# Kernel tuning notes

Measured on AMD Instinct MI355X. Metric: run time of the kernel, lower is better.

Reference implementation:

```python
import jax, jax.numpy as jnp
import numpy as np

V, D, H, NL = 30000, 512, 8, 6
DH = D // H
B, L = 4, 1024
EPS = 1e-5


def setup_inputs() -> dict:
    key = jax.random.key(0)
    ks = jax.random.split(key, 16)
    s = 0.02
    n = lambda k, shape: jax.random.normal(k, shape, jnp.float32) * s
    return {
        'ids': jax.random.randint(ks[0], (B, L), 0, V),
        'embed': n(ks[1], (V, D)),
        'pos_enc': jax.random.normal(ks[2], (1, 1024, D), jnp.float32),
        'rg_w': n(ks[3], (NL, 4, D)), 'rg_b': jnp.zeros((NL, 4), jnp.float32),
        'qkv_w': n(ks[4], (NL, 3 * D, D)), 'qkv_b': jnp.zeros((NL, 3 * D), jnp.float32),
        'out_w': n(ks[5], (NL, D, D)), 'out_b': jnp.zeros((NL, D), jnp.float32),
        'phase_w': n(ks[6], (NL, H, D)), 'phase_b': jnp.zeros((NL, H), jnp.float32),
        'ff1_w': n(ks[7], (NL, 4 * D, D)), 'ff1_b': jnp.zeros((NL, 4 * D), jnp.float32),
        'ff2_w': n(ks[8], (NL, D, 4 * D)), 'ff2_b': jnp.zeros((NL, D), jnp.float32),
        'n1_s': jnp.ones((NL, D), jnp.float32), 'n1_b': jnp.zeros((NL, D), jnp.float32),
        'n2_s': jnp.ones((NL, D), jnp.float32), 'n2_b': jnp.zeros((NL, D), jnp.float32),
        'bnd_w1': n(ks[9], (D, D)), 'bnd_b1': jnp.zeros((D,), jnp.float32),
        'bnd_w2': n(ks[10], (1, D)), 'bnd_b2': jnp.zeros((1,), jnp.float32),
        'head_w': n(ks[11], (V, D)),
    }


def _ln(x, s, b):
    m = x.mean(-1, keepdims=True)
    v = ((x - m) ** 2).mean(-1, keepdims=True)
    return (x - m) * jax.lax.rsqrt(v + EPS) * s + b


def _block(x, p):
    rgw, rgb, qw, qb, ow, ob, pw, pb, f1w, f1b, f2w, f2b, s1, b1, s2, b2 = p
    Bc, Lc, _ = x.shape
    rg = jax.nn.sigmoid(x @ rgw.T + rgb)                       # [B,L,4]
    xm = x * (1.0 + rg.mean(-1, keepdims=True))
    h = _ln(xm, s1, b1)                                        # norm1(x_modulated)
    qkv = (h @ qw.T + qb).reshape(Bc, Lc, 3, H, DH)
    q, k, v = [jnp.transpose(qkv[:, :, i], (0, 2, 1, 3)) for i in range(3)]  # [B,H,L,dh]
    attn = jnp.einsum('bhid,bhjd->bhij', q, k) / (float(DH) ** 0.5)
    phase = jnp.transpose(h @ pw.T + pb, (0, 2, 1))            # [B,H,L]
    bias = -(phase[..., :, None] - phase[..., None, :]) ** 2   # [B,H,L,L]
    attn = jax.nn.softmax(attn + bias, axis=-1)
    ao = jnp.einsum('bhij,bhjd->bhid', attn, v)
    ao = jnp.transpose(ao, (0, 2, 1, 3)).reshape(Bc, Lc, D) @ ow.T + ob
    x = _ln(x + ao, s1, b1)
    ff = jax.nn.gelu(x @ f1w.T + f1b, approximate=False) @ f2w.T + f2b
    x = _ln(x + ff, s2, b2)
    return x, rg


def reference(ids, embed, pos_enc, rg_w, rg_b, qkv_w, qkv_b, out_w, out_b,
              phase_w, phase_b, ff1_w, ff1_b, ff2_w, ff2_b,
              n1_s, n1_b, n2_s, n2_b, bnd_w1, bnd_b1, bnd_w2, bnd_b2, head_w):
    Lc = ids.shape[1]
    x = embed[ids] + pos_enc[:, :Lc, :]
    layer_params = (rg_w, rg_b, qkv_w, qkv_b, out_w, out_b, phase_w, phase_b,
                    ff1_w, ff1_b, ff2_w, ff2_b, n1_s, n1_b, n2_s, n2_b)
    x, rgs = jax.lax.scan(_block, x, layer_params)
    gate = jax.nn.sigmoid((jnp.tanh(x @ bnd_w1.T + bnd_b1) @ bnd_w2.T + bnd_b2)[..., 0])
    logits = (x * gate[..., None]) @ head_w.T
    return logits, gate, rgs[-1]
```

## Files before the change

kernel.cpp:

```cpp
#include <hip/hip_runtime.h>
#include <math.h>

#define D 512
#define NH 8
#define DH 64
#define NL 6
#define Bsz 4
#define Lseq 1024
#define BL 4096
#define Vocab 30000
#define EPS 1e-5f

typedef __attribute__((ext_vector_type(8))) short s8v;
typedef __attribute__((ext_vector_type(4))) float f32x4;
typedef __attribute__((ext_vector_type(4))) float f4v;

__device__ __forceinline__ float sigmoidf_(float x) { return 1.0f / (1.0f + expf(-x)); }

__device__ __forceinline__ short f2bf(float f) {
  union { float f; unsigned u; } v; v.f = f;
  return (short)((v.u + 0x7FFFu + ((v.u >> 16) & 1u)) >> 16);
}
__device__ __forceinline__ float bf2f(short s) {
  union { unsigned u; float f; } v; v.u = ((unsigned)(unsigned short)s) << 16;
  return v.f;
}

__device__ __forceinline__ void gload16(const void* g, void* l) {
  __builtin_amdgcn_global_load_lds(
      (const __attribute__((address_space(1))) void*)g,
      (__attribute__((address_space(3))) void*)l, 16, 0, 0);
}

__device__ __forceinline__ float act_apply(float v, int act) {
  if (act == 1) return 0.5f * v * (1.0f + erff(v * 0.7071067811865475f));
  if (act == 2) return tanhf(v);
  return v;
}

__global__ void f2bf6_kernel(
    const float* __restrict__ s0, short* __restrict__ d0, int n0,
    const float* __restrict__ s1, short* __restrict__ d1, int n1,
    const float* __restrict__ s2, short* __restrict__ d2, int n2,
    const float* __restrict__ s3, short* __restrict__ d3, int n3,
    const float* __restrict__ s4, short* __restrict__ d4, int n4,
    const float* __restrict__ s5, short* __restrict__ d5, int n5) {
  long i = ((long)blockIdx.x * 256 + threadIdx.x) * 8;
  const float* s; short* d;
  if (i < n0) { s = s0; d = d0; }
  else {
    i -= n0;
    if (i < n1) { s = s1; d = d1; }
    else {
      i -= n1;
      if (i < n2) { s = s2; d = d2; }
      else {
        i -= n2;
        if (i < n3) { s = s3; d = d3; }
        else {
          i -= n3;
          if (i < n4) { s = s4; d = d4; }
          else { i -= n4; if (i >= n5) return; s = s5; d = d5; }
        }
      }
    }
  }
  float4 a = *(const float4*)(s + i);
  float4 b = *(const float4*)(s + i + 4);
  s8v o;
  o[0] = f2bf(a.x); o[1] = f2bf(a.y); o[2] = f2bf(a.z); o[3] = f2bf(a.w);
  o[4] = f2bf(b.x); o[5] = f2bf(b.y); o[6] = f2bf(b.z); o[7] = f2bf(b.w);
  *(s8v*)(d + i) = o;
}

__global__ void embed_kernel(const int* __restrict__ ids, const float* __restrict__ emb,
                             const float* __restrict__ pos, float* __restrict__ x) {
  int tok = blockIdx.x;
  int l = tok & (Lseq - 1);
  int id = ids[tok];
  const float4* e = (const float4*)(emb + (size_t)id * D);
  const float4* p = (const float4*)(pos + (size_t)l * D);
  float4* o = (float4*)(x + (size_t)tok * D);
  float4 a = e[threadIdx.x], b = p[threadIdx.x];
  o[threadIdx.x] = make_float4(a.x + b.x, a.y + b.y, a.z + b.z, a.w + b.w);
}

__global__ __launch_bounds__(256) void rg_ln_kernel(
    const float* __restrict__ x, const float* __restrict__ rgw, const float* __restrict__ rgb,
    const float* __restrict__ sc, const float* __restrict__ bi,
    const float* __restrict__ pw, const float* __restrict__ pb,
    short* __restrict__ h, float* __restrict__ phase, float* __restrict__ rg_out) {
  __shared__ float smg[4][4];
  __shared__ float sms[4][2];
  __shared__ float smp[4][8];
  int tok = blockIdx.x, t = threadIdx.x, wid = t >> 6, lane = t & 63;
  const float* xr = x + (size_t)tok * D;
  float x0 = xr[t], x1 = xr[t + 256];
  float p0 = x0 * rgw[t]        + x1 * rgw[t + 256];
  float p1 = x0 * rgw[512 + t]  + x1 * rgw[512 + t + 256];
  float p2 = x0 * rgw[1024 + t] + x1 * rgw[1024 + t + 256];
  float p3 = x0 * rgw[1536 + t] + x1 * rgw[1536 + t + 256];
#pragma unroll
  for (int off = 32; off > 0; off >>= 1) {
    p0 += __shfl_xor(p0, off, 64);
    p1 += __shfl_xor(p1, off, 64);
    p2 += __shfl_xor(p2, off, 64);
    p3 += __shfl_xor(p3, off, 64);
  }
  if (lane == 0) { smg[wid][0] = p0; smg[wid][1] = p1; smg[wid][2] = p2; smg[wid][3] = p3; }
  __syncthreads();
  float g0 = sigmoidf_(smg[0][0] + smg[1][0] + smg[2][0] + smg[3][0] + rgb[0]);
  float g1 = sigmoidf_(smg[0][1] + smg[1][1] + smg[2][1] + smg[3][1] + rgb[1]);
  float g2 = sigmoidf_(smg[0][2] + smg[1][2] + smg[2][2] + smg[3][2] + rgb[2]);
  float g3 = sigmoidf_(smg[0][3] + smg[1][3] + smg[2][3] + smg[3][3] + rgb[3]);
  if (rg_out != nullptr && t == 0) {
    float* ro = rg_out + (size_t)tok * 4;
    ro[0] = g0; ro[1] = g1; ro[2] = g2; ro[3] = g3;
  }
  float mod = 1.0f + 0.25f * (g0 + g1 + g2 + g3);
  float m0 = x0 * mod, m1 = x1 * mod;
  float s = m0 + m1, q = m0 * m0 + m1 * m1;
#pragma unroll
  for (int off = 32; off > 0; off >>= 1) {
    s += __shfl_xor(s, off, 64);
    q += __shfl_xor(q, off, 64);
  }
  if (lane == 0) { sms[wid][0] = s; sms[wid][1] = q; }
  __syncthreads();
  float S = sms[0][0] + sms[1][0] + sms[2][0] + sms[3][0];
  float Q = sms[0][1] + sms[1][1] + sms[2][1] + sms[3][1];
  float mean = S * (1.0f / D);
  float var = Q * (1.0f / D) - mean * mean;
  float rstd = rsqrtf(var + EPS);
  float o0 = (m0 - mean) * rstd * sc[t] + bi[t];
  float o1 = (m1 - mean) * rstd * sc[t + 256] + bi[t + 256];
  h[(size_t)tok * D + t] = f2bf(o0);
  h[(size_t)tok * D + t + 256] = f2bf(o1);
  float ph[8];
#pragma unroll
  for (int hh = 0; hh < 8; hh++) {
    ph[hh] = o0 * pw[hh * D + t] + o1 * pw[hh * D + t + 256];
#pragma unroll
    for (int off = 32; off > 0; off >>= 1) ph[hh] += __shfl_xor(ph[hh], off, 64);
  }
  if (lane == 0) {
#pragma unroll
    for (int hh = 0; hh < 8; hh++) smp[wid][hh] = ph[hh];
  }
  __syncthreads();
  if (t < 8)
    phase[(size_t)tok * NH + t] = smp[0][t] + smp[1][t] + smp[2][t] + smp[3][t] + pb[t];
}

__global__ __launch_bounds__(256) void residual_ln_kernel(
    float* __restrict__ x, const short* __restrict__ y,
    const float* __restrict__ sc, const float* __restrict__ bi,
    short* __restrict__ xb) {
  __shared__ float sms[4][2];
  int tok = blockIdx.x, t = threadIdx.x, wid = t >> 6, lane = t & 63;
  float v0 = x[(size_t)tok * D + t] + bf2f(y[(size_t)tok * D + t]);
  float v1 = x[(size_t)tok * D + t + 256] + bf2f(y[(size_t)tok * D + t + 256]);
  float s = v0 + v1, q = v0 * v0 + v1 * v1;
#pragma unroll
  for (int off = 32; off > 0; off >>= 1) {
    s += __shfl_xor(s, off, 64);
    q += __shfl_xor(q, off, 64);
  }
  if (lane == 0) { sms[wid][0] = s; sms[wid][1] = q; }
  __syncthreads();
  float S = sms[0][0] + sms[1][0] + sms[2][0] + sms[3][0];
  float Q = sms[0][1] + sms[1][1] + sms[2][1] + sms[3][1];
  float mean = S * (1.0f / D);
  float var = Q * (1.0f / D) - mean * mean;
  float rstd = rsqrtf(var + EPS);
  float o0 = (v0 - mean) * rstd * sc[t] + bi[t];
  float o1 = (v1 - mean) * rstd * sc[t + 256] + bi[t + 256];
  x[(size_t)tok * D + t] = o0;
  x[(size_t)tok * D + t + 256] = o1;
  xb[(size_t)tok * D + t] = f2bf(o0);
  xb[(size_t)tok * D + t + 256] = f2bf(o1);
}

template <int MODE, bool SWAP>
__global__ __launch_bounds__(256) void gemm128_kernel(
    const short* __restrict__ A, const short* __restrict__ W,
    const float* __restrict__ bias, float* __restrict__ C,
    int M, int N, int K, int act) {
  __shared__ char smem[32768];
  short* AsF = (short*)smem;
  short* WsF = (short*)(smem + 16384);
  int tid = threadIdx.x;
  int bn, bm;
  if (SWAP) { bm = blockIdx.x * 128; bn = blockIdx.y * 128; }
  else      { bn = blockIdx.x * 128; bm = blockIdx.y * 128; }
  int wid = tid >> 6, lane = tid & 63;
  int wm = (wid >> 1) * 64, wn = (wid & 1) * 64;
  int fr = lane & 15, kg = lane >> 4;
  f32x4 acc[4][4] = {};
  int srow = 32 * wid + (lane >> 2);
  int scol = (lane & 3) * 8;
  const short* Ag0 = A + (size_t)(bm + srow) * K + scol;
  const short* Ag1 = Ag0 + (size_t)16 * K;
  int wr0 = bn + srow;       if (wr0 >= N) wr0 = N - 1;
  int wr1 = bn + srow + 16;  if (wr1 >= N) wr1 = N - 1;
  const short* Wg0 = W + (size_t)wr0 * K + scol;
  const short* Wg1 = W + (size_t)wr1 * K + scol;
  auto stage = [&](int buf, int k0) {
    gload16(Ag0 + k0, AsF + buf * 4096 + (32 * wid) * 32);
    gload16(Ag1 + k0, AsF + buf * 4096 + (32 * wid + 16) * 32);
    gload16(Wg0 + k0, WsF + buf * 4096 + (32 * wid) * 32);
    gload16(Wg1 + k0, WsF + buf * 4096 + (32 * wid + 16) * 32);
  };
  stage(0, 0);
  __syncthreads();
  int nt = K / 32, cur = 0;
  for (int t = 0; t < nt; ++t) {
    if (t + 1 < nt) stage(cur ^ 1, (t + 1) * 32);
    const short* ab = AsF + cur * 4096;
    const short* wb = WsF + cur * 4096;
    s8v af[4], bfv[4];
#pragma unroll
    for (int m = 0; m < 4; m++) af[m] = *(const s8v*)(ab + (wm + m * 16 + fr) * 32 + kg * 8);
#pragma unroll
    for (int n = 0; n < 4; n++) bfv[n] = *(const s8v*)(wb + (wn + n * 16 + fr) * 32 + kg * 8);
#pragma unroll
    for (int m = 0; m < 4; m++)
#pragma unroll
      for (int n = 0; n < 4; n++)
        acc[m][n] = __builtin_amdgcn_mfma_f32_16x16x32_bf16(af[m], bfv[n], acc[m][n], 0, 0, 0);
    __syncthreads();
    cur ^= 1;
  }
  float* eps = (float*)smem;
#pragma unroll
  for (int c = 0; c < 2; ++c) {
    __syncthreads();
    if ((wid >> 1) == c) {
#pragma unroll
      for (int n = 0; n < 4; n++) {
        int col = wn + n * 16 + fr;
        int gcol = bn + col;
        float bv = bias ? bias[gcol < N ? gcol : N - 1] : 0.0f;
#pragma unroll
        for (int m = 0; m < 4; m++)
#pragma unroll
          for (int r = 0; r < 4; r++)
            eps[(m * 16 + kg * 4 + r) * 128 + col] = act_apply(acc[m][n][r] + bv, act);
      }
    }
    __syncthreads();
#pragma unroll
    for (int i = 0; i < 8; i++) {
      int idx = tid + i * 256;
      int rl = idx >> 5;
      int c4 = (idx & 31) * 4;
      int row = bm + c * 64 + rl;
      int col = bn + c4;
      f4v v = *(f4v*)&eps[rl * 128 + c4];
      float* dst = C + (size_t)row * N + col;
      if (col + 3 < N) {
        if (MODE == 1) __builtin_nontemporal_store(v, (f4v*)dst);
        else *(f4v*)dst = v;
      } else {
        for (int j = 0; j < 4; j++)
          if (col + j < N) {
            if (MODE == 1) __builtin_nontemporal_store(v[j], dst + j);
            else dst[j] = v[j];
          }
      }
    }
  }
}

template <bool OUTBF>
__global__ __launch_bounds__(256) void gemm64_kernel(
    const short* __restrict__ A, const short* __restrict__ W,
    const float* __restrict__ bias, float* __restrict__ C, short* __restrict__ Cb,
    short* __restrict__ Vt, int M, int N, int K, int act) {
  __shared__ char smem[24576];
  short* AsF = (short*)smem;
  short* WsF = (short*)(smem + 8192);
  int tid = threadIdx.x;
  int bn = blockIdx.x * 128, bm = blockIdx.y * 64;
  int wid = tid >> 6, lane = tid & 63;
  int fr = lane & 15, kg = lane >> 4;
  f32x4 acc[4][2] = {};
  int l4 = lane >> 2;
  int scol = (lane & 3) * 8;
  const short* Ag0 = A + (size_t)(bm + 16 * wid + l4) * K + scol;
  int wr0 = bn + 32 * wid + l4;       if (wr0 >= N) wr0 = N - 1;
  int wr1 = bn + 32 * wid + 16 + l4;  if (wr1 >= N) wr1 = N - 1;
  const short* Wg0 = W + (size_t)wr0 * K + scol;
  const short* Wg1 = W + (size_t)wr1 * K + scol;
  auto stage = [&](int buf, int k0) {
    gload16(Ag0 + k0, AsF + buf * 2048 + (16 * wid) * 32);
    gload16(Wg0 + k0, WsF + buf * 4096 + (32 * wid) * 32);
    gload16(Wg1 + k0, WsF + buf * 4096 + (32 * wid + 16) * 32);
  };
  stage(0, 0);
  __syncthreads();
  int nt = K / 32, cur = 0;
  for (int t = 0; t < nt; ++t) {
    if (t + 1 < nt) stage(cur ^ 1, (t + 1) * 32);
    const short* ab = AsF + cur * 2048;
    const short* wb = WsF + cur * 4096;
    s8v af[4], bfv[2];
#pragma unroll
    for (int m = 0; m < 4; m++) af[m] = *(const s8v*)(ab + (m * 16 + fr) * 32 + kg * 8);
#pragma unroll
    for (int n = 0; n < 2; n++) bfv[n] = *(const s8v*)(wb + (wid * 32 + n * 16 + fr) * 32 + kg * 8);
#pragma unroll
    for (int m = 0; m < 4; m++)
#pragma unroll
      for (int n = 0; n < 2; n++)
        acc[m][n] = __builtin_amdgcn_mfma_f32_16x16x32_bf16(af[m], bfv[n], acc[m][n], 0, 0, 0);
    __syncthreads();
    cur ^= 1;
  }
  int rbase = bm + kg * 4;
  if (Vt != nullptr && bn >= 1024) {
#pragma unroll
    for (int n = 0; n < 2; n++) {
      int col = bn + wid * 32 + n * 16 + fr;
      float bv = bias ? bias[col] : 0.0f;
      int hh = (col - 1024) >> 6, dd = (col - 1024) & 63;
#pragma unroll
      for (int m = 0; m < 4; m++) {
        int row0 = rbase + m * 16;
        int bb = row0 >> 10, ll = row0 & 1023;
        short4 pk;
        pk.x = f2bf(acc[m][n][0] + bv);
        pk.y = f2bf(acc[m][n][1] + bv);
        pk.z = f2bf(acc[m][n][2] + bv);
        pk.w = f2bf(acc[m][n][3] + bv);
        *(short4*)&Vt[((((size_t)bb * NH + hh) * DH + dd) << 10) | ll] = pk;
      }
    }
    return;
  }
  if (OUTBF) {
    short* eph = (short*)smem;
    __syncthreads();
#pragma unroll
    for (int n = 0; n < 2; n++) {
      int col = wid * 32 + n * 16 + fr;
      float bv = bias ? bias[bn + col] : 0.0f;
#pragma unroll
      for (int m = 0; m < 4; m++)
#pragma unroll
        for (int r = 0; r < 4; r++)
          eph[(kg * 4 + m * 16 + r) * 128 + col] = f2bf(act_apply(acc[m][n][r] + bv, act));
    }
    __syncthreads();
#pragma unroll
    for (int i = 0; i < 4; i++) {
      int idx = tid + i * 256;
      int rl = idx >> 4;
      int c8 = (idx & 15) * 8;
      *(s8v*)&Cb[(size_t)(bm + rl) * N + bn + c8] = *(s8v*)&eph[rl * 128 + c8];
    }
  } else {
#pragma unroll
    for (int n = 0; n < 2; n++) {
      int col = bn + wid * 32 + n * 16 + fr;
      if (col >= N) continue;
      float bv = bias ? bias[col] : 0.0f;
#pragma unroll
      for (int m = 0; m < 4; m++)
#pragma unroll
        for (int r = 0; r < 4; r++)
          C[(size_t)(rbase + m * 16 + r) * N + col] = act_apply(acc[m][n][r] + bv, act);
    }
  }
}

template <bool OUTBF>
__global__ __launch_bounds__(256) void gemm_conv_kernel(
    const short* __restrict__ A, const float* __restrict__ Wp,
    const float* __restrict__ bias, float* __restrict__ C, short* __restrict__ Cb,
    short* __restrict__ Vt, int M, int N, int K, int act) {
  __shared__ short As[128][40];
  __shared__ short Ws[128][40];
  int tid = threadIdx.x;
  int bn = blockIdx.x * 128, bm = blockIdx.y * 128;
  int wid = tid >> 6, lane = tid & 63;
  int wm = (wid >> 1) * 64, wn = (wid & 1) * 64;
  int fr = lane & 15, kg = lane >> 4;
  f32x4 acc[4][4] = {};
  int sr = tid >> 1;
  int sc = (tid & 1) * 16;
  const short* Arow = A + (size_t)(bm + sr) * K + sc;
  int wrow = bn + sr;
  int wclamp = wrow < N ? wrow : 0;
  const float* Wrow_f = Wp + (size_t)wclamp * K + sc;
  for (int k0 = 0; k0 < K; k0 += 32) {
    s8v a0 = *(const s8v*)(Arow + k0);
    s8v a1 = *(const s8v*)(Arow + k0 + 8);
    s8v w0, w1;
    float4 f0 = *(const float4*)(Wrow_f + k0);
    float4 f1 = *(const float4*)(Wrow_f + k0 + 4);
    float4 f2 = *(const float4*)(Wrow_f + k0 + 8);
    float4 f3 = *(const float4*)(Wrow_f + k0 + 12);
    w0[0] = f2bf(f0.x); w0[1] = f2bf(f0.y); w0[2] = f2bf(f0.z); w0[3] = f2bf(f0.w);
    w0[4] = f2bf(f1.x); w0[5] = f2bf(f1.y); w0[6] = f2bf(f1.z); w0[7] = f2bf(f1.w);
    w1[0] = f2bf(f2.x); w1[1] = f2bf(f2.y); w1[2] = f2bf(f2.z); w1[3] = f2bf(f2.w);
    w1[4] = f2bf(f3.x); w1[5] = f2bf(f3.y); w1[6] = f2bf(f3.z); w1[7] = f2bf(f3.w);
    __syncthreads();
    *(s8v*)&As[sr][sc] = a0;
    *(s8v*)&As[sr][sc + 8] = a1;
    *(s8v*)&Ws[sr][sc] = w0;
    *(s8v*)&Ws[sr][sc + 8] = w1;
    __syncthreads();
    s8v af[4], bfv[4];
#pragma unroll
    for (int m = 0; m < 4; m++) af[m] = *(const s8v*)&As[wm + m * 16 + fr][kg * 8];
#pragma unroll
    for (int n = 0; n < 4; n++) bfv[n] = *(const s8v*)&Ws[wn + n * 16 + fr][kg * 8];
#pragma unroll
    for (int m = 0; m < 4; m++)
#pragma unroll
      for (int n = 0; n < 4; n++)
        acc[m][n] = __builtin_amdgcn_mfma_f32_16x16x32_bf16(af[m], bfv[n], acc[m][n], 0, 0, 0);
  }
  int rbase = bm + wm + kg * 4;
#pragma unroll
  for (int n = 0; n < 4; n++) {
    int col = bn + wn + n * 16 + fr;
    if (col >= N) continue;
    float bv = bias ? bias[col] : 0.0f;
    if (Vt != nullptr && col >= 1024) {
      int hh = (col - 1024) >> 6, dd = (col - 1024) & 63;
#pragma unroll
      for (int m = 0; m < 4; m++) {
        int row0 = rbase + m * 16;
        int bb = row0 >> 10, ll = row0 & 1023;
        short4 pk;
        pk.x = f2bf(acc[m][n][0] + bv);
        pk.y = f2bf(acc[m][n][1] + bv);
        pk.z = f2bf(acc[m][n][2] + bv);
        pk.w = f2bf(acc[m][n][3] + bv);
        *(short4*)&Vt[((((size_t)bb * NH + hh) * DH + dd) << 10) | ll] = pk;
      }
      continue;
    }
#pragma unroll
    for (int m = 0; m < 4; m++) {
#pragma unroll
      for (int r = 0; r < 4; r++) {
        int row = rbase + m * 16 + r;
        float v = act_apply(acc[m][n][r] + bv, act);
        if (OUTBF) Cb[(size_t)row * N + col] = f2bf(v);
        else C[(size_t)row * N + col] = v;
      }
    }
  }
}

__global__ __launch_bounds__(256) void mha_kernel(
    const short* __restrict__ qkv, const short* __restrict__ vt,
    const float* __restrict__ phase, short* __restrict__ out) {
  __shared__ short sQ[64][72];
  __shared__ short sK[64][72];
  __shared__ short sVt[64][72];
  __shared__ short sP[64][72];
  __shared__ float sPh[Lseq];
  int bh = blockIdx.y;
  int b = bh >> 3, h = bh & 7;
  int q0 = blockIdx.x * 64;
  int tid = threadIdx.x;
  int lane = tid & 63, wid = tid >> 6;
  int fr = lane & 15, kg = lane >> 4;
  int wm = wid * 16;
  const short* vtb = vt + ((size_t)bh * DH) * Lseq;

  for (int j = tid; j < Lseq; j += 256) sPh[j] = phase[((size_t)(b * Lseq + j)) * NH + h];
  for (int idx = tid; idx < 512; idx += 256) {
    int row = idx >> 3, c8 = (idx & 7) * 8;
    *(s8v*)&sQ[row][c8] =
        *(const s8v*)(qkv + (((size_t)(b * Lseq + q0 + row)) * 3 + 0) * D + h * DH + c8);
  }
  __syncthreads();

  float phq[4];
#pragma unroll
  for (int r = 0; r < 4; r++) phq[r] = sPh[q0 + wm + kg * 4 + r];

  float mrow[4] = {-1e30f, -1e30f, -1e30f, -1e30f};
  float lrow[4] = {0.f, 0.f, 0.f, 0.f};
  f32x4 o[4] = {};

  for (int kt = 0; kt < Lseq / 64; kt++) {
    int k0 = kt * 64;
    __syncthreads();
    for (int idx = tid; idx < 512; idx += 256) {
      int row = idx >> 3, c8 = (idx & 7) * 8;
      *(s8v*)&sK[row][c8] =
          *(const s8v*)(qkv + (((size_t)(b * Lseq + k0 + row)) * 3 + 1) * D + h * DH + c8);
      *(s8v*)&sVt[row][c8] = *(const s8v*)(vtb + (size_t)row * Lseq + k0 + c8);
    }
    __syncthreads();

    s8v qa0 = *(const s8v*)&sQ[wm + fr][kg * 8];
    s8v qa1 = *(const s8v*)&sQ[wm + fr][32 + kg * 8];
    f32x4 sacc[4];
#pragma unroll
    for (int n = 0; n < 4; n++) {
      f32x4 z = {};
      s8v kb0 = *(const s8v*)&sK[n * 16 + fr][kg * 8];
      s8v kb1 = *(const s8v*)&sK[n * 16 + fr][32 + kg * 8];
      z = __builtin_amdgcn_mfma_f32_16x16x32_bf16(qa0, kb0, z, 0, 0, 0);
      z = __builtin_amdgcn_mfma_f32_16x16x32_bf16(qa1, kb1, z, 0, 0, 0);
      sacc[n] = z;
    }
    float sv[4][4];
#pragma unroll
    for (int n = 0; n < 4; n++) {
      float phk = sPh[k0 + n * 16 + fr];
#pragma unroll
      for (int r = 0; r < 4; r++) {
        float dp = phq[r] - phk;
        sv[n][r] = sacc[n][r] * 0.125f - dp * dp;
      }
    }
    float mnew[4], alpha[4];
#pragma unroll
    for (int r = 0; r < 4; r++) {
      float mx = fmaxf(fmaxf(sv[0][r], sv[1][r]), fmaxf(sv[2][r], sv[3][r]));
#pragma unroll
      for (int off = 1; off < 16; off <<= 1) mx = fmaxf(mx, __shfl_xor(mx, off, 64));
      mnew[r] = fmaxf(mrow[r], mx);
      alpha[r] = __expf(mrow[r] - mnew[r]);
      mrow[r] = mnew[r];
    }
    float rs[4] = {0.f, 0.f, 0.f, 0.f};
#pragma unroll
    for (int n = 0; n < 4; n++) {
#pragma unroll
      for (int r = 0; r < 4; r++) {
        float p = __expf(sv[n][r] - mnew[r]);
        rs[r] += p;
        sP[wm + kg * 4 + r][n * 16 + fr] = f2bf(p);
      }
    }
#pragma unroll
    for (int r = 0; r < 4; r++) {
#pragma unroll
      for (int off = 1; off < 16; off <<= 1) rs[r] += __shfl_xor(rs[r], off, 64);
      lrow[r] = lrow[r] * alpha[r] + rs[r];
    }
#pragma unroll
    for (int df = 0; df < 4; df++) {
      o[df][0] *= alpha[0]; o[df][1] *= alpha[1];
      o[df][2] *= alpha[2]; o[df][3] *= alpha[3];
    }
    s8v pa0 = *(const s8v*)&sP[wm + fr][kg * 8];
    s8v pa1 = *(const s8v*)&sP[wm + fr][32 + kg * 8];
#pragma unroll
    for (int df = 0; df < 4; df++) {
      int d = df * 16 + fr;
      s8v vb0 = *(const s8v*)&sVt[d][kg * 8];
      s8v vb1 = *(const s8v*)&sVt[d][32 + kg * 8];
      o[df] = __builtin_amdgcn_mfma_f32_16x16x32_bf16(pa0, vb0, o[df], 0, 0, 0);
      o[df] = __builtin_amdgcn_mfma_f32_16x16x32_bf16(pa1, vb1, o[df], 0, 0, 0);
    }
  }
  float inv[4];
#pragma unroll
  for (int r = 0; r < 4; r++) inv[r] = 1.0f / lrow[r];
#pragma unroll
  for (int df = 0; df < 4; df++) {
#pragma unroll
    for (int r = 0; r < 4; r++) {
      int row = q0 + wm + kg * 4 + r;
      out[((size_t)(b * Lseq + row)) * D + h * DH + df * 16 + fr] = f2bf(o[df][r] * inv[r]);
    }
  }
}

__global__ __launch_bounds__(128) void gatexg_kernel(
    const float* __restrict__ tb, const float* __restrict__ w2,
    const float* __restrict__ b2, const float* __restrict__ x,
    float* __restrict__ gate, short* __restrict__ xg) {
  __shared__ float sred[2];
  int tok = blockIdx.x, t = threadIdx.x;
  const float* row = tb + (size_t)tok * D;
  float acc = row[t] * w2[t] + row[t + 128] * w2[t + 128] +
              row[t + 256] * w2[t + 256] + row[t + 384] * w2[t + 384];
#pragma unroll
  for (int off = 32; off > 0; off >>= 1) acc += __shfl_xor(acc, off, 64);
  if ((t & 63) == 0) sred[t >> 6] = acc;
  __syncthreads();
  float g = 1.0f / (1.0f + expf(-(sred[0] + sred[1] + b2[0])));
  if (t == 0) gate[tok] = g;
  float4 v = *(const float4*)(x + (size_t)tok * D + t * 4);
  short4 o = make_short4(f2bf(v.x * g), f2bf(v.y * g), f2bf(v.z * g), f2bf(v.w * g));
  *(short4*)(xg + (size_t)tok * D + t * 4) = o;
}

extern "C" void kernel_launch(void* const* d_in, const int* in_sizes, int n_in,
                              void* d_out, int out_size, void* d_ws, size_t ws_size,
                              hipStream_t stream) {
  const int* ids = (const int*)d_in[0];
  const float* emb = (const float*)d_in[1];
  const float* pos = (const float*)d_in[2];
  const float* rg_w = (const float*)d_in[3];
  const float* rg_b = (const float*)d_in[4];
  const float* qkv_w = (const float*)d_in[5];
  const float* qkv_b = (const float*)d_in[6];
  const float* out_w = (const float*)d_in[7];
  const float* out_b = (const float*)d_in[8];
  const float* ph_w = (const float*)d_in[9];
  const float* ph_b = (const float*)d_in[10];
  const float* ff1_w = (const float*)d_in[11];
  const float* ff1_b = (const float*)d_in[12];
  const float* ff2_w = (const float*)d_in[13];
  const float* ff2_b = (const float*)d_in[14];
  const float* n1_s = (const float*)d_in[15];
  const float* n1_b = (const float*)d_in[16];
  const float* n2_s = (const float*)d_in[17];
  const float* n2_b = (const float*)d_in[18];
  const float* bw1 = (const float*)d_in[19];
  const float* bb1 = (const float*)d_in[20];
  const float* bw2 = (const float*)d_in[21];
  const float* bb2 = (const float*)d_in[22];
  const float* head_w = (const float*)d_in[23];

  char* w = (char*)d_ws;
  float* x      = (float*)(w + 0);
  float* ao     = (float*)(w + 8388608);
  short* y_bf   = (short*)(w + 8388608);
  float* phase  = (float*)(w + 16777216);
  short* h_bf   = (short*)(w + 16908288);
  short* ao_bf  = (short*)(w + 21102592);
  short* x_bf   = (short*)(w + 25296896);
  short* ff_bf  = (short*)(w + 29491200);
  short* xg_bf  = (short*)(w + 46268416);
  short* qkv_bf = (short*)(w + 50462720);
  short* vt_bf  = (short*)(w + 63045632);
  short* wqkv   = (short*)(w + 67239936);
  short* wout   = (short*)(w + 76677120);
  short* wff1   = (short*)(w + 79822848);
  short* wff2   = (short*)(w + 92405760);
  short* wbnd   = (short*)(w + 104988672);
  short* whead  = (short*)(w + 105512960);
  const size_t WS_FULL = 136232960;

  float* outf   = (float*)d_out;
  float* logits = outf;
  float* gate   = outf + 122880000;
  float* rg_out = outf + 122884096;

  bool fast = ws_size >= WS_FULL;

  if (fast) {
    f2bf6_kernel<<<(34496512 / 8 + 255) / 256, 256, 0, stream>>>(
        qkv_w, wqkv, 4718592, out_w, wout, 1572864, ff1_w, wff1, 6291456,
        ff2_w, wff2, 6291456, bw1, wbnd, 262144, head_w, whead, 15360000);
  }

  embed_kernel<<<BL, 128, 0, stream>>>(ids, emb, pos, x);

  for (int l = 0; l < NL; l++) {
    rg_ln_kernel<<<BL, 256, 0, stream>>>(
        x, rg_w + (size_t)l * 4 * D, rg_b + l * 4, n1_s + l * D, n1_b + l * D,
        ph_w + (size_t)l * NH * D, ph_b + l * NH,
        h_bf, phase, (l == NL - 1) ? rg_out : nullptr);
    if (fast)
      gemm64_kernel<true><<<dim3(12, 64), 256, 0, stream>>>(
          h_bf, wqkv + (size_t)l * 1536 * D, qkv_b + l * 1536, nullptr, qkv_bf, vt_bf,
          BL, 1536, D, 0);
    else
      gemm_conv_kernel<true><<<dim3(12, 32), 256, 0, stream>>>(
          h_bf, qkv_w + (size_t)l * 1536 * D, qkv_b + l * 1536, nullptr, qkv_bf, vt_bf,
          BL, 1536, D, 0);
    mha_kernel<<<dim3(Lseq / 64, Bsz * NH), 256, 0, stream>>>(qkv_bf, vt_bf, phase, ao_bf);
    if (fast)
      gemm64_kernel<true><<<dim3(4, 64), 256, 0, stream>>>(
          ao_bf, wout + (size_t)l * D * D, out_b + l * D, nullptr, y_bf, nullptr, BL, D, D, 0);
    else
      gemm_conv_kernel<true><<<dim3(4, 32), 256, 0, stream>>>(
          ao_bf, out_w + (size_t)l * D * D, out_b + l * D, nullptr, y_bf, nullptr, BL, D, D, 0);
    residual_ln_kernel<<<BL, 256, 0, stream>>>(x, y_bf, n1_s + l * D, n1_b + l * D, x_bf);
    if (fast)
      gemm64_kernel<true><<<dim3(16, 64), 256, 0, stream>>>(
          x_bf, wff1 + (size_t)l * 2048 * D, ff1_b + l * 2048, nullptr, ff_bf, nullptr,
          BL, 2048, D, 1);
    else
      gemm_conv_kernel<true><<<dim3(16, 32), 256, 0, stream>>>(
          x_bf, ff1_w + (size_t)l * 2048 * D, ff1_b + l * 2048, nullptr, ff_bf, nullptr,
          BL, 2048, D, 1);
    if (fast)
      gemm64_kernel<true><<<dim3(4, 64), 256, 0, stream>>>(
          ff_bf, wff2 + (size_t)l * D * 2048, ff2_b + l * D, nullptr, y_bf, nullptr,
          BL, D, 2048, 0);
    else
      gemm_conv_kernel<true><<<dim3(4, 32), 256, 0, stream>>>(
          ff_bf, ff2_w + (size_t)l * D * 2048, ff2_b + l * D, nullptr, y_bf, nullptr,
          BL, D, 2048, 0);
    residual_ln_kernel<<<BL, 256, 0, stream>>>(x, y_bf, n2_s + l * D, n2_b + l * D, x_bf);
  }

  if (fast)
    gemm64_kernel<false><<<dim3(4, 64), 256, 0, stream>>>(
        x_bf, wbnd, bb1, ao, nullptr, nullptr, BL, D, D, 2);
  else
    gemm_conv_kernel<false><<<dim3(4, 32), 256, 0, stream>>>(
        x_bf, bw1, bb1, ao, nullptr, nullptr, BL, D, D, 2);
  gatexg_kernel<<<BL, 128, 0, stream>>>(ao, bw2, bb2, x, gate, xg_bf);
  if (fast)
    gemm128_kernel<1, true><<<dim3(32, 235), 256, 0, stream>>>(
        xg_bf, whead, nullptr, logits, BL, Vocab, D, 0);
  else
    gemm_conv_kernel<false><<<dim3(235, 32), 256, 0, stream>>>(
        xg_bf, head_w, nullptr, logits, nullptr, nullptr, BL, Vocab, D, 0);
}
```

Measured before the change: 1.220 ms.

## Prefetch next K/V tile into registers in attention; restructure phase projection

The attention kernel now loads the next 64-row K and V^T tiles into registers while the current tile is being computed, then stores them to shared memory at the top of the next iteration. This hides global-load latency behind the MFMA work. Separately, the phase projection in rg_ln stages the normalized row in shared memory so each wave computes two heads with vectorized loads, replacing eight full-block reductions. The cost is extra registers in the attention kernel, which could lower occupancy.

```diff
diff --git a/kernel.cpp b/kernel.cpp
--- a/kernel.cpp
+++ b/kernel.cpp
@@ -92,7 +92,7 @@
     short* __restrict__ h, float* __restrict__ phase, float* __restrict__ rg_out) {
   __shared__ float smg[4][4];
   __shared__ float sms[4][2];
-  __shared__ float smp[4][8];
+  __shared__ float smh[512];
   int tok = blockIdx.x, t = threadIdx.x, wid = t >> 6, lane = t & 63;
   const float* xr = x + (size_t)tok * D;
   float x0 = xr[t], x1 = xr[t + 256];
@@ -136,20 +136,28 @@
   float o1 = (m1 - mean) * rstd * sc[t + 256] + bi[t + 256];
   h[(size_t)tok * D + t] = f2bf(o0);
   h[(size_t)tok * D + t + 256] = f2bf(o1);
-  float ph[8];
-#pragma unroll
-  for (int hh = 0; hh < 8; hh++) {
-    ph[hh] = o0 * pw[hh * D + t] + o1 * pw[hh * D + t + 256];
-#pragma unroll
-    for (int off = 32; off > 0; off >>= 1) ph[hh] += __shfl_xor(ph[hh], off, 64);
+  smh[t] = o0;
+  smh[t + 256] = o1;
+  __syncthreads();
+  const float4* hv = (const float4*)&smh[lane * 8];
+  float4 a0 = hv[0], a1 = hv[1];
+  float ph[2];
+#pragma unroll
+  for (int j = 0; j < 2; j++) {
+    int hh = wid * 2 + j;
+    const float4* wv = (const float4*)&pw[hh * D + lane * 8];
+    float4 b0 = wv[0], b1 = wv[1];
+    float acc = a0.x * b0.x + a0.y * b0.y + a0.z * b0.z + a0.w * b0.w +
+                a1.x * b1.x + a1.y * b1.y + a1.z * b1.z + a1.w * b1.w;
+#pragma unroll
+    for (int off = 32; off > 0; off >>= 1) acc += __shfl_xor(acc, off, 64);
+    ph[j] = acc;
   }
   if (lane == 0) {
-#pragma unroll
-    for (int hh = 0; hh < 8; hh++) smp[wid][hh] = ph[hh];
-  }
-  __syncthreads();
-  if (t < 8)
-    phase[(size_t)tok * NH + t] = smp[0][t] + smp[1][t] + smp[2][t] + smp[3][t] + pb[t];
+    int hh = wid * 2;
+    phase[(size_t)tok * NH + hh] = ph[0] + pb[hh];
+    phase[(size_t)tok * NH + hh + 1] = ph[1] + pb[hh + 1];
+  }
 }
 
 __global__ __launch_bounds__(256) void residual_ln_kernel(
@@ -473,12 +481,25 @@
   int wm = wid * 16;
   const short* vtb = vt + ((size_t)bh * DH) * Lseq;
 
+  int srow0 = tid >> 3, srow1 = (tid + 256) >> 3;
+  int sc8_0 = (tid & 7) * 8, sc8_1 = sc8_0;
+  const short* kbase = qkv + ((size_t)(b * Lseq) * 3 + 1) * D + h * DH;
+
   for (int j = tid; j < Lseq; j += 256) sPh[j] = phase[((size_t)(b * Lseq + j)) * NH + h];
   for (int idx = tid; idx < 512; idx += 256) {
     int row = idx >> 3, c8 = (idx & 7) * 8;
     *(s8v*)&sQ[row][c8] =
         *(const s8v*)(qkv + (((size_t)(b * Lseq + q0 + row)) * 3 + 0) * D + h * DH + c8);
   }
+
+  s8v kr0, kr1, vr0, vr1;
+  auto loadkv = [&](int k0) {
+    kr0 = *(const s8v*)(kbase + (size_t)(k0 + srow0) * 3 * D + sc8_0);
+    kr1 = *(const s8v*)(kbase + (size_t)(k0 + srow1) * 3 * D + sc8_1);
+    vr0 = *(const s8v*)(vtb + (size_t)srow0 * Lseq + k0 + sc8_0);
+    vr1 = *(const s8v*)(vtb + (size_t)srow1 * Lseq + k0 + sc8_1);
+  };
+  loadkv(0);
   __syncthreads();
 
   float phq[4];
@@ -492,13 +513,12 @@
   for (int kt = 0; kt < Lseq / 64; kt++) {
     int k0 = kt * 64;
     __syncthreads();
-    for (int idx = tid; idx < 512; idx += 256) {
-      int row = idx >> 3, c8 = (idx & 7) * 8;
-      *(s8v*)&sK[row][c8] =
-          *(const s8v*)(qkv + (((size_t)(b * Lseq + k0 + row)) * 3 + 1) * D + h * DH + c8);
-      *(s8v*)&sVt[row][c8] = *(const s8v*)(vtb + (size_t)row * Lseq + k0 + c8);
-    }
-    __syncthreads();
+    *(s8v*)&sK[srow0][sc8_0] = kr0;
+    *(s8v*)&sK[srow1][sc8_1] = kr1;
+    *(s8v*)&sVt[srow0][sc8_0] = vr0;
+    *(s8v*)&sVt[srow1][sc8_1] = vr1;
+    __syncthreads();
+    if (kt + 1 < Lseq / 64) loadkv(k0 + 64);
 
     s8v qa0 = *(const s8v*)&sQ[wm + fr][kg * 8];
     s8v qa1 = *(const s8v*)&sQ[wm + fr][32 + kg * 8];
```

Result: faster. 1.154 ms (-5.5%).
